# Optimization experiments

Hardware: AMD Instinct MI355X
Metric: run time of the kernel (lower is better)

The kernel has to match this reference:

```python
import jax, jax.numpy as jnp
import numpy as np

B, L, K = 2, 1024, 30
NUM_RBF = 16
MAX_REL = 32  # max_relative_feature
POS_DIM = 16

# atom order in stacked table: N=0, Ca=1, C=2, O=3, Cb=4
_PAIRS = [(0,0),(2,2),(3,3),(4,4),(1,0),(1,2),(1,3),(1,4),(0,2),(0,3),(0,4),
          (4,2),(4,3),(3,2),(0,1),(2,1),(3,1),(4,1),(2,0),(3,0),(4,0),(2,4),(3,4),(2,3)]


def setup_inputs() -> dict:
    key = jax.random.key(0)
    ks = jax.random.split(key, 6)
    X = jax.random.normal(ks[0], (B, L, 4, 3), dtype=jnp.float32) * 3.0
    chain_idx = jnp.sort(jax.random.randint(ks[1], (B, L), 0, 4), axis=-1)
    mask = jnp.ones((B, L), dtype=jnp.float32)
    E_idx = jax.random.randint(ks[2], (B, L, K), 0, L)
    D_neighbors = jax.random.uniform(ks[3], (B, L, K), dtype=jnp.float32) * 22.0
    W_pos = jax.random.normal(ks[4], (POS_DIM, 2 * MAX_REL + 2), dtype=jnp.float32) * 0.1
    b_pos = jax.random.normal(ks[5], (POS_DIM,), dtype=jnp.float32) * 0.01
    return {"X": X, "chain_idx": chain_idx, "mask": mask, "E_idx": E_idx,
            "D_neighbors": D_neighbors, "W_pos": W_pos, "b_pos": b_pos}


def _rbf(D):
    # D: [..., ] -> [..., NUM_RBF]
    D_mu = jnp.linspace(2.0, 22.0, NUM_RBF, dtype=D.dtype)
    D_sigma = (22.0 - 2.0) / NUM_RBF
    return jnp.exp(-(((D[..., None] - D_mu) / D_sigma) ** 2))


def _residue_idx(chain_idx):
    # faithful to the torch loop: chains 0..n-2 get 100*(chain#) + global pos, last chain stays -100
    boundary = jnp.concatenate(
        [jnp.zeros((chain_idx.shape[0], 1), jnp.int32),
         (chain_idx[:, 1:] != chain_idx[:, :-1]).astype(jnp.int32)], axis=1)
    chain_num = jnp.cumsum(boundary, axis=1)              # [B,L]
    last = chain_num[:, -1:]
    pos = jnp.arange(chain_idx.shape[1], dtype=jnp.int32)[None, :]
    return jnp.where(chain_num < last, 100 * chain_num + pos, -100)


def _forward(X, chain_idx, mask, E_idx, D_neighbors, W_pos, b_pos):
    N, Ca, C, O = X[:, :, 0], X[:, :, 1], X[:, :, 2], X[:, :, 3]
    b = Ca - N
    c = C - Ca
    a = jnp.cross(b, c)
    Cb = -0.58273431 * a + 0.56802827 * b - 0.54067466 * c + Ca
    atoms = jnp.stack([N, Ca, C, O, Cb], axis=0)          # [5,B,L,3]

    ia = jnp.array([p[0] for p in _PAIRS])
    ib = jnp.array([p[1] for p in _PAIRS])

    def pair_rbf(A_pts, B_pts):
        # full pairwise distance then gather down to top-k neighbors (faithful to original)
        dX = A_pts[:, :, None, :] - B_pts[:, None, :, :]   # [B,L,L,3]
        D = jnp.sqrt(jnp.sum(dX ** 2, axis=-1) + 1e-6)     # [B,L,L]
        Dn = jnp.take_along_axis(D, E_idx, axis=2)         # [B,L,K]
        return _rbf(Dn)                                     # [B,L,K,16]

    RBF_pairs = jax.vmap(pair_rbf)(atoms[ia], atoms[ib])   # [24,B,L,K,16]
    RBF_pairs = jnp.transpose(RBF_pairs, (1, 2, 3, 0, 4)).reshape(
        X.shape[0], X.shape[1], E_idx.shape[2], 24 * NUM_RBF)
    RBF_all = jnp.concatenate([_rbf(D_neighbors), RBF_pairs], axis=-1)  # [B,L,K,400]

    ridx = _residue_idx(chain_idx)                          # [B,L] int32
    offset = ridx[:, :, None] - ridx[:, None, :]            # [B,L,L]
    offset = jnp.take_along_axis(offset, E_idx, axis=2)     # [B,L,K]
    d_chains = (chain_idx[:, :, None] == chain_idx[:, None, :]).astype(jnp.int32)
    E_chains = jnp.take_along_axis(d_chains, E_idx, axis=2)  # [B,L,K]

    d = jnp.clip(offset + MAX_REL, 0, 2 * MAX_REL) * E_chains + (1 - E_chains) * (2 * MAX_REL + 1)
    d_onehot = jax.nn.one_hot(d, 2 * MAX_REL + 2, dtype=W_pos.dtype)   # [B,L,K,66]
    E_positional = jnp.einsum('blkc,ec->blke', d_onehot, W_pos) + b_pos

    return jnp.concatenate([E_positional, RBF_all], axis=-1)  # [B,L,K,416]


def reference(X, chain_idx, mask, E_idx, D_neighbors, W_pos, b_pos):
    return _forward(X, chain_idx, mask, E_idx, D_neighbors, W_pos, b_pos)
```

## Files before the change

### kernel.cpp

```cpp
#include <hip/hip_runtime.h>

#define BB 2
#define LL 1024
#define KK 30
#define NCH 416
#define PER_BLOCK (KK * NCH)
#define NF4 (PER_BLOCK / 4)

__device__ __constant__ unsigned char PAIR_A[24] =
    {0,2,3,4,1,1,1,1,0,0,0,4,4,3,0,2,3,4,2,3,4,2,3,2};
__device__ __constant__ unsigned char PAIR_B[24] =
    {0,2,3,4,0,2,3,4,2,3,4,2,3,2,1,1,1,1,0,0,0,4,4,3};

__global__ __launch_bounds__(256)
void feat_fused(const float* __restrict__ X, const int* __restrict__ chainG,
                const int* __restrict__ E_idx, const float* __restrict__ D_neighbors,
                const float* __restrict__ W_pos, const float* __restrict__ b_pos,
                float* __restrict__ out)
{
    __shared__ float Wlds[16 * 66];
    __shared__ float bpos[16];
    __shared__ float latm[16];
    __shared__ float natm[KK][16];
    __shared__ float pd[KK][26];
    __shared__ int   dd[KK];
    __shared__ int   iaib[24];
    __shared__ int   wmask[4];

    const int tid = threadIdx.x;
    const int bi  = blockIdx.x;
    const int l   = bi & (LL - 1);
    const int rowbase = bi - l;

    const int4 cv = reinterpret_cast<const int4*>(chainG + rowbase)[tid];
    int pm = (1 << cv.x) | (1 << cv.y) | (1 << cv.z) | (1 << cv.w);
    #pragma unroll
    for (int off = 32; off >= 1; off >>= 1) pm |= __shfl_xor(pm, off, 64);
    if ((tid & 63) == 0) wmask[tid >> 6] = pm;

    for (int i = tid; i < 16 * 66; i += 256) Wlds[i] = W_pos[i];
    if (tid < 16) bpos[tid] = b_pos[tid];
    if (tid < 24) iaib[tid] = ((int)(3 * PAIR_A[tid]) << 8) | (int)(3 * PAIR_B[tid]);

    int jj = 0, chj = 0;
    if (tid < KK) {
        jj  = E_idx[bi * KK + tid];
        chj = chainG[rowbase + jj];
        pd[tid][0] = D_neighbors[bi * KK + tid] * 0.8f;
    }
    if (tid <= KK) {
        const int j = (tid < KK) ? (rowbase + jj) : bi;
        const float4* xp = reinterpret_cast<const float4*>(X + (size_t)j * 12);
        const float4 x0 = xp[0], x1 = xp[1], x2 = xp[2];
        const float bx = x0.w - x0.x, by = x1.x - x0.y, bz = x1.y - x0.z;
        const float cx = x1.z - x0.w, cy = x1.w - x1.x, cz = x2.x - x1.y;
        const float ax = by * cz - bz * cy;
        const float ay = bz * cx - bx * cz;
        const float az = bx * cy - by * cx;
        const float ka = -0.58273431f, kb = 0.56802827f, kc = -0.54067466f;
        float* ap = (tid < KK) ? &natm[tid][0] : &latm[0];
        ap[0]  = x0.x; ap[1]  = x0.y; ap[2]  = x0.z;
        ap[3]  = x0.w; ap[4]  = x1.x; ap[5]  = x1.y;
        ap[6]  = x1.z; ap[7]  = x1.w; ap[8]  = x2.x;
        ap[9]  = x2.y; ap[10] = x2.z; ap[11] = x2.w;
        ap[12] = ka * ax + kb * bx + kc * cx + x0.w;
        ap[13] = ka * ay + kb * by + kc * cy + x1.x;
        ap[14] = ka * az + kb * bz + kc * cz + x1.y;
    }
    __syncthreads();

    if (tid < KK) {
        const int mask = wmask[0] | wmask[1] | wmask[2] | wmask[3];
        const int chl  = chainG[bi];
        const int npres = __popc(mask);
        const int cl1 = __popc(mask & ((2 << chl) - 1));
        const int cj1 = __popc(mask & ((2 << chj) - 1));
        const int rl = (cl1 < npres) ? (100 * (cl1 - 1) + l)  : -100;
        const int rj = (cj1 < npres) ? (100 * (cj1 - 1) + jj) : -100;
        int off = rl - rj + 32;
        off = off < 0 ? 0 : (off > 64 ? 64 : off);
        dd[tid] = (chl == chj) ? off : 65;
    }

    for (int i = tid; i < KK * 24; i += 256) {
        const int k  = i / 24;
        const int p  = i - k * 24;
        const int pk = iaib[p];
        const int ao = pk >> 8;
        const int bo = pk & 255;
        const float dx = latm[ao]     - natm[k][bo];
        const float dy = latm[ao + 1] - natm[k][bo + 1];
        const float dz = latm[ao + 2] - natm[k][bo + 2];
        const float D  = sqrtf(dx * dx + dy * dy + dz * dz + 1e-6f);
        pd[k][1 + p] = D * 0.8f;
    }
    __syncthreads();

    float* outp = out + (size_t)bi * PER_BLOCK;
    const float MU0    = 1.6f;
    const float MUSTEP = 1.0666666666666667f;
    const float NLOG2E = -1.44269504088896f;

    for (int i4 = tid; i4 < NF4; i4 += 256) {
        const int k  = i4 / 104;
        const int c0 = (i4 - k * 104) * 4;
        float4 v;
        if (c0 < 16) {
            const int d = dd[k];
            v.x = Wlds[(c0 + 0) * 66 + d] + bpos[c0 + 0];
            v.y = Wlds[(c0 + 1) * 66 + d] + bpos[c0 + 1];
            v.z = Wlds[(c0 + 2) * 66 + d] + bpos[c0 + 2];
            v.w = Wlds[(c0 + 3) * 66 + d] + bpos[c0 + 3];
        } else {
            const int q  = (c0 - 16) >> 4;
            const int m0 = (c0 - 16) & 15;
            const float D8 = pd[k][q];
            const float t0 = D8 - (MU0 + (float)(m0 + 0) * MUSTEP);
            const float t1 = D8 - (MU0 + (float)(m0 + 1) * MUSTEP);
            const float t2 = D8 - (MU0 + (float)(m0 + 2) * MUSTEP);
            const float t3 = D8 - (MU0 + (float)(m0 + 3) * MUSTEP);
            v.x = __builtin_amdgcn_exp2f(t0 * t0 * NLOG2E);
            v.y = __builtin_amdgcn_exp2f(t1 * t1 * NLOG2E);
            v.z = __builtin_amdgcn_exp2f(t2 * t2 * NLOG2E);
            v.w = __builtin_amdgcn_exp2f(t3 * t3 * NLOG2E);
        }
        *reinterpret_cast<float4*>(outp + i4 * 4) = v;
    }
}

extern "C" void kernel_launch(void* const* d_in, const int* in_sizes, int n_in,
                              void* d_out, int out_size, void* d_ws, size_t ws_size,
                              hipStream_t stream)
{
    const float* X           = (const float*)d_in[0];
    const int*   chain_idx   = (const int*)  d_in[1];
    const int*   E_idx       = (const int*)  d_in[3];
    const float* D_neighbors = (const float*)d_in[4];
    const float* W_pos       = (const float*)d_in[5];
    const float* b_pos       = (const float*)d_in[6];
    float* out = (float*)d_out;

    feat_fused<<<BB * LL, 256, 0, stream>>>(X, chain_idx, E_idx, D_neighbors,
                                            W_pos, b_pos, out);
}
```

Before: 25.12 us.

## Process two residue positions per block and split positional/RBF output loops

Each block now handles two consecutive positions, which halves the grid and amortizes the per-block setup (W_pos load, chain mask reduction) across twice the output. The chain array is cached in shared memory, and the bias is folded into the W table when it is loaded. The positional-embedding stores are split out from the RBF loop, which removes the per-element branch. The cost is more setup work and shared memory per block, fewer blocks in flight, and a dead leftover read of dd.

```diff
diff --git a/kernel.cpp b/kernel.cpp
--- a/kernel.cpp
+++ b/kernel.cpp
@@ -4,127 +4,185 @@
 #define LL 1024
 #define KK 30
 #define NCH 416
-#define PER_BLOCK (KK * NCH)
-#define NF4 (PER_BLOCK / 4)
+#define PER_POS (KK * NCH)
+#define RBF4 3000
+#define POS4 120
 
 __device__ __constant__ unsigned char PAIR_A[24] =
     {0,2,3,4,1,1,1,1,0,0,0,4,4,3,0,2,3,4,2,3,4,2,3,2};
 __device__ __constant__ unsigned char PAIR_B[24] =
     {0,2,3,4,0,2,3,4,2,3,4,2,3,2,1,1,1,1,0,0,0,4,4,3};
 
+__device__ __forceinline__ void build_atoms(float* ap, float4 x0, float4 x1, float4 x2)
+{
+    const float bx = x0.w - x0.x, by = x1.x - x0.y, bz = x1.y - x0.z;
+    const float cx = x1.z - x0.w, cy = x1.w - x1.x, cz = x2.x - x1.y;
+    const float ax = by * cz - bz * cy;
+    const float ay = bz * cx - bx * cz;
+    const float az = bx * cy - by * cx;
+    const float ka = -0.58273431f, kb = 0.56802827f, kc = -0.54067466f;
+    ap[0]  = x0.x; ap[1]  = x0.y; ap[2]  = x0.z;
+    ap[3]  = x0.w; ap[4]  = x1.x; ap[5]  = x1.y;
+    ap[6]  = x1.z; ap[7]  = x1.w; ap[8]  = x2.x;
+    ap[9]  = x2.y; ap[10] = x2.z; ap[11] = x2.w;
+    ap[12] = ka * ax + kb * bx + kc * cx + x0.w;
+    ap[13] = ka * ay + kb * by + kc * cy + x1.x;
+    ap[14] = ka * az + kb * bz + kc * cz + x1.y;
+}
+
 __global__ __launch_bounds__(256)
-void feat_fused(const float* __restrict__ X, const int* __restrict__ chainG,
-                const int* __restrict__ E_idx, const float* __restrict__ D_neighbors,
-                const float* __restrict__ W_pos, const float* __restrict__ b_pos,
-                float* __restrict__ out)
+void feat_fused2(const float* __restrict__ X, const int* __restrict__ chainG,
+                 const int* __restrict__ E_idx, const float* __restrict__ D_neighbors,
+                 const float* __restrict__ W_pos, const float* __restrict__ b_pos,
+                 float* __restrict__ out)
 {
-    __shared__ float Wlds[16 * 66];
-    __shared__ float bpos[16];
-    __shared__ float latm[16];
-    __shared__ float natm[KK][16];
-    __shared__ float pd[KK][26];
-    __shared__ int   dd[KK];
+    __shared__ float Wst[16 * 66];
+    __shared__ int   schain[LL];
+    __shared__ float latm[2][16];
+    __shared__ float natm[2][KK][16];
+    __shared__ float pd[2][KK][26];
+    __shared__ int   dd[2][KK];
     __shared__ int   iaib[24];
     __shared__ int   wmask[4];
 
     const int tid = threadIdx.x;
-    const int bi  = blockIdx.x;
-    const int l   = bi & (LL - 1);
-    const int rowbase = bi - l;
-
-    const int4 cv = reinterpret_cast<const int4*>(chainG + rowbase)[tid];
-    int pm = (1 << cv.x) | (1 << cv.y) | (1 << cv.z) | (1 << cv.w);
+    const int p0  = blockIdx.x * 2;
+    const int p1  = p0 + 1;
+    const int l0  = p0 & (LL - 1);
+    const int l1  = l0 + 1;
+    const int rowbase = p0 - l0;
+
+    const int4 cvv = reinterpret_cast<const int4*>(chainG + rowbase)[tid];
+    reinterpret_cast<int4*>(schain)[tid] = cvv;
+    int pm = (1 << cvv.x) | (1 << cvv.y) | (1 << cvv.z) | (1 << cvv.w);
     #pragma unroll
     for (int off = 32; off >= 1; off >>= 1) pm |= __shfl_xor(pm, off, 64);
     if ((tid & 63) == 0) wmask[tid >> 6] = pm;
 
-    for (int i = tid; i < 16 * 66; i += 256) Wlds[i] = W_pos[i];
-    if (tid < 16) bpos[tid] = b_pos[tid];
+    for (int i = tid; i < 16 * 66; i += 256) Wst[i] = W_pos[i] + b_pos[i / 66];
     if (tid < 24) iaib[tid] = ((int)(3 * PAIR_A[tid]) << 8) | (int)(3 * PAIR_B[tid]);
 
-    int jj = 0, chj = 0;
+    int jj0 = 0, jj1 = 0;
     if (tid < KK) {
-        jj  = E_idx[bi * KK + tid];
-        chj = chainG[rowbase + jj];
-        pd[tid][0] = D_neighbors[bi * KK + tid] * 0.8f;
+        jj0 = E_idx[p0 * KK + tid];
+        jj1 = E_idx[p1 * KK + tid];
+        pd[0][tid][0] = D_neighbors[p0 * KK + tid] * 0.8f;
+        pd[1][tid][0] = D_neighbors[p1 * KK + tid] * 0.8f;
     }
     if (tid <= KK) {
-        const int j = (tid < KK) ? (rowbase + jj) : bi;
-        const float4* xp = reinterpret_cast<const float4*>(X + (size_t)j * 12);
-        const float4 x0 = xp[0], x1 = xp[1], x2 = xp[2];
-        const float bx = x0.w - x0.x, by = x1.x - x0.y, bz = x1.y - x0.z;
-        const float cx = x1.z - x0.w, cy = x1.w - x1.x, cz = x2.x - x1.y;
-        const float ax = by * cz - bz * cy;
-        const float ay = bz * cx - bx * cz;
-        const float az = bx * cy - by * cx;
-        const float ka = -0.58273431f, kb = 0.56802827f, kc = -0.54067466f;
-        float* ap = (tid < KK) ? &natm[tid][0] : &latm[0];
-        ap[0]  = x0.x; ap[1]  = x0.y; ap[2]  = x0.z;
-        ap[3]  = x0.w; ap[4]  = x1.x; ap[5]  = x1.y;
-        ap[6]  = x1.z; ap[7]  = x1.w; ap[8]  = x2.x;
-        ap[9]  = x2.y; ap[10] = x2.z; ap[11] = x2.w;
-        ap[12] = ka * ax + kb * bx + kc * cx + x0.w;
-        ap[13] = ka * ay + kb * by + kc * cy + x1.x;
-        ap[14] = ka * az + kb * bz + kc * cz + x1.y;
+        const int j0 = (tid < KK) ? (rowbase + jj0) : p0;
+        const int j1 = (tid < KK) ? (rowbase + jj1) : p1;
+        const float4* q0 = reinterpret_cast<const float4*>(X + (size_t)j0 * 12);
+        const float4* q1 = reinterpret_cast<const float4*>(X + (size_t)j1 * 12);
+        const float4 a0 = q0[0], a1 = q0[1], a2 = q0[2];
+        const float4 b0 = q1[0], b1 = q1[1], b2 = q1[2];
+        build_atoms((tid < KK) ? &natm[0][tid][0] : &latm[0][0], a0, a1, a2);
+        build_atoms((tid < KK) ? &natm[1][tid][0] : &latm[1][0], b0, b1, b2);
     }
     __syncthreads();
 
     if (tid < KK) {
-        const int mask = wmask[0] | wmask[1] | wmask[2] | wmask[3];
-        const int chl  = chainG[bi];
+        const int mask  = wmask[0] | wmask[1] | wmask[2] | wmask[3];
         const int npres = __popc(mask);
-        const int cl1 = __popc(mask & ((2 << chl) - 1));
-        const int cj1 = __popc(mask & ((2 << chj) - 1));
-        const int rl = (cl1 < npres) ? (100 * (cl1 - 1) + l)  : -100;
-        const int rj = (cj1 < npres) ? (100 * (cj1 - 1) + jj) : -100;
-        int off = rl - rj + 32;
-        off = off < 0 ? 0 : (off > 64 ? 64 : off);
-        dd[tid] = (chl == chj) ? off : 65;
-    }
-
-    for (int i = tid; i < KK * 24; i += 256) {
-        const int k  = i / 24;
-        const int p  = i - k * 24;
-        const int pk = iaib[p];
-        const int ao = pk >> 8;
-        const int bo = pk & 255;
-        const float dx = latm[ao]     - natm[k][bo];
-        const float dy = latm[ao + 1] - natm[k][bo + 1];
-        const float dz = latm[ao + 2] - natm[k][bo + 2];
+        {
+            const int chl = schain[l0], chj = schain[jj0];
+            const int cl1 = __popc(mask & ((2 << chl) - 1));
+            const int cj1 = __popc(mask & ((2 << chj) - 1));
+            const int rl = (cl1 < npres) ? (100 * (cl1 - 1) + l0)  : -100;
+            const int rj = (cj1 < npres) ? (100 * (cj1 - 1) + jj0) : -100;
+            int off = rl - rj + 32;
+            off = off < 0 ? 0 : (off > 64 ? 64 : off);
+            dd[0][tid] = (chl == chj) ? off : 65;
+        }
+        {
+            const int chl = schain[l1], chj = schain[jj1];
+            const int cl1 = __popc(mask & ((2 << chl) - 1));
+            const int cj1 = __popc(mask & ((2 << chj) - 1));
+            const int rl = (cl1 < npres) ? (100 * (cl1 - 1) + l1)  : -100;
+            const int rj = (cj1 < npres) ? (100 * (cj1 - 1) + jj1) : -100;
+            int off = rl - rj + 32;
+            off = off < 0 ? 0 : (off > 64 ? 64 : off);
+            dd[1][tid] = (chl == chj) ? off : 65;
+        }
+    }
+
+    for (int i = tid; i < 2 * KK * 24; i += 256) {
+        const int g   = (i >= KK * 24);
+        const int rem = i - g * (KK * 24);
+        const int k   = rem / 24;
+        const int p   = rem - k * 24;
+        const int pk  = iaib[p];
+        const int ao  = pk >> 8;
+        const int bo  = pk & 255;
+        const float dx = latm[g][ao]     - natm[g][k][bo];
+        const float dy = latm[g][ao + 1] - natm[g][k][bo + 1];
+        const float dz = latm[g][ao + 2] - natm[g][k][bo + 2];
         const float D  = sqrtf(dx * dx + dy * dy + dz * dz + 1e-6f);
-        pd[k][1 + p] = D * 0.8f;
+        pd[g][k][1 + p] = D * 0.8f;
     }
     __syncthreads();
 
-    float* outp = out + (size_t)bi * PER_BLOCK;
+    float* outp0 = out + (size_t)p0 * PER_POS;
+    float* outp1 = outp0 + PER_POS;
+
+    if (tid < 2 * POS4) {
+        const int g   = (tid >= POS4);
+        const int rem = tid - g * POS4;
+        const int k   = rem >> 2;
+        const int c0  = (rem & 3) * 4;
+        const int d   = dd[g][tid >> 2 & 31];
+        (void)d;
+        const int dv  = dd[g][k];
+        float4 v;
+        v.x = Wst[(c0 + 0) * 66 + dv];
+        v.y = Wst[(c0 + 1) * 66 + dv];
+        v.z = Wst[(c0 + 2) * 66 + dv];
+        v.w = Wst[(c0 + 3) * 66 + dv];
+        float* op = g ? outp1 : outp0;
+        *reinterpret_cast<float4*>(op + k * NCH + c0) = v;
+    }
+
     const float MU0    = 1.6f;
     const float MUSTEP = 1.0666666666666667f;
     const float NLOG2E = -1.44269504088896f;
 
-    for (int i4 = tid; i4 < NF4; i4 += 256) {
-        const int k  = i4 / 104;
-        const int c0 = (i4 - k * 104) * 4;
+    #pragma unroll 1
+    for (int i4 = tid; i4 < RBF4; i4 += 256) {
+        const int k    = i4 / 100;
+        const int rem4 = i4 - k * 100;
+        const int q    = rem4 >> 2;
+        const int m0   = (rem4 & 3) << 2;
+        const float D8 = pd[0][k][q];
+        const float mu = MU0 + (float)m0 * MUSTEP;
+        const float t0 = D8 - mu;
+        const float t1 = D8 - (mu + MUSTEP);
+        const float t2 = D8 - (mu + 2.0f * MUSTEP);
+        const float t3 = D8 - (mu + 3.0f * MUSTEP);
         float4 v;
-        if (c0 < 16) {
-            const int d = dd[k];
-            v.x = Wlds[(c0 + 0) * 66 + d] + bpos[c0 + 0];
-            v.y = Wlds[(c0 + 1) * 66 + d] + bpos[c0 + 1];
-            v.z = Wlds[(c0 + 2) * 66 + d] + bpos[c0 + 2];
-            v.w = Wlds[(c0 + 3) * 66 + d] + bpos[c0 + 3];
-        } else {
-            const int q  = (c0 - 16) >> 4;
-            const int m0 = (c0 - 16) & 15;
-            const float D8 = pd[k][q];
-            const float t0 = D8 - (MU0 + (float)(m0 + 0) * MUSTEP);
-            const float t1 = D8 - (MU0 + (float)(m0 + 1) * MUSTEP);
-            const float t2 = D8 - (MU0 + (float)(m0 + 2) * MUSTEP);
-            const float t3 = D8 - (MU0 + (float)(m0 + 3) * MUSTEP);
-            v.x = __builtin_amdgcn_exp2f(t0 * t0 * NLOG2E);
-            v.y = __builtin_amdgcn_exp2f(t1 * t1 * NLOG2E);
-            v.z = __builtin_amdgcn_exp2f(t2 * t2 * NLOG2E);
-            v.w = __builtin_amdgcn_exp2f(t3 * t3 * NLOG2E);
-        }
-        *reinterpret_cast<float4*>(outp + i4 * 4) = v;
+        v.x = __builtin_amdgcn_exp2f(t0 * t0 * NLOG2E);
+        v.y = __builtin_amdgcn_exp2f(t1 * t1 * NLOG2E);
+        v.z = __builtin_amdgcn_exp2f(t2 * t2 * NLOG2E);
+        v.w = __builtin_amdgcn_exp2f(t3 * t3 * NLOG2E);
+        *reinterpret_cast<float4*>(outp0 + k * NCH + 16 + rem4 * 4) = v;
+    }
+    #pragma unroll 1
+    for (int i4 = tid; i4 < RBF4; i4 += 256) {
+        const int k    = i4 / 100;
+        const int rem4 = i4 - k * 100;
+        const int q    = rem4 >> 2;
+        const int m0   = (rem4 & 3) << 2;
+        const float D8 = pd[1][k][q];
+        const float mu = MU0 + (float)m0 * MUSTEP;
+        const float t0 = D8 - mu;
+        const float t1 = D8 - (mu + MUSTEP);
+        const float t2 = D8 - (mu + 2.0f * MUSTEP);
+        const float t3 = D8 - (mu + 3.0f * MUSTEP);
+        float4 v;
+        v.x = __builtin_amdgcn_exp2f(t0 * t0 * NLOG2E);
+        v.y = __builtin_amdgcn_exp2f(t1 * t1 * NLOG2E);
+        v.z = __builtin_amdgcn_exp2f(t2 * t2 * NLOG2E);
+        v.w = __builtin_amdgcn_exp2f(t3 * t3 * NLOG2E);
+        *reinterpret_cast<float4*>(outp1 + k * NCH + 16 + rem4 * 4) = v;
     }
 }
 
@@ -140,6 +198,6 @@
     const float* b_pos       = (const float*)d_in[6];
     float* out = (float*)d_out;
 
-    feat_fused<<<BB * LL, 256, 0, stream>>>(X, chain_idx, E_idx, D_neighbors,
-                                            W_pos, b_pos, out);
+    feat_fused2<<<(BB * LL) / 2, 256, 0, stream>>>(X, chain_idx, E_idx,
+                                                   D_neighbors, W_pos, b_pos, out);
 }
```

After: 26.02 us. 3.6% more time.

## Split each position's neighbors across six blocks to raise parallelism

Applied to the files above, without the earlier changes.

Each block now handles 5 of the 30 neighbors for one position instead of all 30, so the grid grows sixfold and each block's output loop becomes three fixed emits. The bias is folded into the staged W table, removing one add per positional output. The cost is that every block repeats the per-row work: loading W_pos into shared memory, the chain-mask reduction over 1024 chain ids, and building the center residue's atoms.

```diff
diff --git a/kernel.cpp b/kernel.cpp
--- a/kernel.cpp
+++ b/kernel.cpp
@@ -4,75 +4,84 @@
 #define LL 1024
 #define KK 30
 #define NCH 416
-#define PER_BLOCK (KK * NCH)
-#define NF4 (PER_BLOCK / 4)
+#define PER_POS (KK * NCH)
+#define KC 5
+#define NBPP (KK / KC)
+#define WF4 (KC * 104)
 
 __device__ __constant__ unsigned char PAIR_A[24] =
     {0,2,3,4,1,1,1,1,0,0,0,4,4,3,0,2,3,4,2,3,4,2,3,2};
 __device__ __constant__ unsigned char PAIR_B[24] =
     {0,2,3,4,0,2,3,4,2,3,4,2,3,2,1,1,1,1,0,0,0,4,4,3};
 
+__device__ __forceinline__ void build_atoms(float* ap, float4 x0, float4 x1, float4 x2)
+{
+    const float bx = x0.w - x0.x, by = x1.x - x0.y, bz = x1.y - x0.z;
+    const float cx = x1.z - x0.w, cy = x1.w - x1.x, cz = x2.x - x1.y;
+    const float ax = by * cz - bz * cy;
+    const float ay = bz * cx - bx * cz;
+    const float az = bx * cy - by * cx;
+    const float ka = -0.58273431f, kb = 0.56802827f, kc = -0.54067466f;
+    ap[0]  = x0.x; ap[1]  = x0.y; ap[2]  = x0.z;
+    ap[3]  = x0.w; ap[4]  = x1.x; ap[5]  = x1.y;
+    ap[6]  = x1.z; ap[7]  = x1.w; ap[8]  = x2.x;
+    ap[9]  = x2.y; ap[10] = x2.z; ap[11] = x2.w;
+    ap[12] = ka * ax + kb * bx + kc * cx + x0.w;
+    ap[13] = ka * ay + kb * by + kc * cy + x1.x;
+    ap[14] = ka * az + kb * bz + kc * cz + x1.y;
+}
+
 __global__ __launch_bounds__(256)
-void feat_fused(const float* __restrict__ X, const int* __restrict__ chainG,
+void feat_split(const float* __restrict__ X, const int* __restrict__ chainG,
                 const int* __restrict__ E_idx, const float* __restrict__ D_neighbors,
                 const float* __restrict__ W_pos, const float* __restrict__ b_pos,
                 float* __restrict__ out)
 {
-    __shared__ float Wlds[16 * 66];
-    __shared__ float bpos[16];
+    __shared__ float Wst[16 * 66];
     __shared__ float latm[16];
-    __shared__ float natm[KK][16];
-    __shared__ float pd[KK][26];
-    __shared__ int   dd[KK];
+    __shared__ float natm[KC][16];
+    __shared__ float pd[KC][26];
+    __shared__ int   dd[KC];
     __shared__ int   iaib[24];
     __shared__ int   wmask[4];
 
     const int tid = threadIdx.x;
-    const int bi  = blockIdx.x;
-    const int l   = bi & (LL - 1);
-    const int rowbase = bi - l;
+    const int bid = blockIdx.x;
+    const int pos = bid / NBPP;
+    const int kc  = bid - pos * NBPP;
+    const int k0  = kc * KC;
+    const int l   = pos & (LL - 1);
+    const int rowbase = pos - l;
 
-    const int4 cv = reinterpret_cast<const int4*>(chainG + rowbase)[tid];
-    int pm = (1 << cv.x) | (1 << cv.y) | (1 << cv.z) | (1 << cv.w);
-    #pragma unroll
-    for (int off = 32; off >= 1; off >>= 1) pm |= __shfl_xor(pm, off, 64);
-    if ((tid & 63) == 0) wmask[tid >> 6] = pm;
+    int jj = 0, chj = 0;
+    if (tid < KC) {
+        jj  = E_idx[pos * KK + k0 + tid];
+        chj = chainG[rowbase + jj];
+        pd[tid][0] = D_neighbors[pos * KK + k0 + tid] * 0.8f;
+    }
+    if (tid <= KC) {
+        const int j = (tid < KC) ? (rowbase + jj) : pos;
+        const float4* xp = reinterpret_cast<const float4*>(X + (size_t)j * 12);
+        const float4 x0 = xp[0], x1 = xp[1], x2 = xp[2];
+        build_atoms((tid < KC) ? &natm[tid][0] : &latm[0], x0, x1, x2);
+    }
 
-    for (int i = tid; i < 16 * 66; i += 256) Wlds[i] = W_pos[i];
-    if (tid < 16) bpos[tid] = b_pos[tid];
+    for (int i = tid; i < 16 * 66; i += 256) Wst[i] = W_pos[i] + b_pos[i / 66];
     if (tid < 24) iaib[tid] = ((int)(3 * PAIR_A[tid]) << 8) | (int)(3 * PAIR_B[tid]);
 
-    int jj = 0, chj = 0;
-    if (tid < KK) {
-        jj  = E_idx[bi * KK + tid];
-        chj = chainG[rowbase + jj];
-        pd[tid][0] = D_neighbors[bi * KK + tid] * 0.8f;
-    }
-    if (tid <= KK) {
-        const int j = (tid < KK) ? (rowbase + jj) : bi;
-        const float4* xp = reinterpret_cast<const float4*>(X + (size_t)j * 12);
-        const float4 x0 = xp[0], x1 = xp[1], x2 = xp[2];
-        const float bx = x0.w - x0.x, by = x1.x - x0.y, bz = x1.y - x0.z;
-        const float cx = x1.z - x0.w, cy = x1.w - x1.x, cz = x2.x - x1.y;
-        const float ax = by * cz - bz * cy;
-        const float ay = bz * cx - bx * cz;
-        const float az = bx * cy - by * cx;
-        const float ka = -0.58273431f, kb = 0.56802827f, kc = -0.54067466f;
-        float* ap = (tid < KK) ? &natm[tid][0] : &latm[0];
-        ap[0]  = x0.x; ap[1]  = x0.y; ap[2]  = x0.z;
-        ap[3]  = x0.w; ap[4]  = x1.x; ap[5]  = x1.y;
-        ap[6]  = x1.z; ap[7]  = x1.w; ap[8]  = x2.x;
-        ap[9]  = x2.y; ap[10] = x2.z; ap[11] = x2.w;
-        ap[12] = ka * ax + kb * bx + kc * cx + x0.w;
-        ap[13] = ka * ay + kb * by + kc * cy + x1.x;
-        ap[14] = ka * az + kb * bz + kc * cz + x1.y;
+    {
+        const int4 cv = reinterpret_cast<const int4*>(chainG + rowbase)[tid];
+        int pm = (1 << cv.x) | (1 << cv.y) | (1 << cv.z) | (1 << cv.w);
+        #pragma unroll
+        for (int off = 32; off >= 1; off >>= 1) pm |= __shfl_xor(pm, off, 64);
+        if ((tid & 63) == 0) wmask[tid >> 6] = pm;
     }
     __syncthreads();
 
-    if (tid < KK) {
-        const int mask = wmask[0] | wmask[1] | wmask[2] | wmask[3];
-        const int chl  = chainG[bi];
+    if (tid < KC) {
+        const int mask  = wmask[0] | wmask[1] | wmask[2] | wmask[3];
         const int npres = __popc(mask);
+        const int chl   = chainG[pos];
         const int cl1 = __popc(mask & ((2 << chl) - 1));
         const int cj1 = __popc(mask & ((2 << chj) - 1));
         const int rl = (cl1 < npres) ? (100 * (cl1 - 1) + l)  : -100;
@@ -82,9 +91,9 @@
         dd[tid] = (chl == chj) ? off : 65;
     }
 
-    for (int i = tid; i < KK * 24; i += 256) {
-        const int k  = i / 24;
-        const int p  = i - k * 24;
+    if (tid < KC * 24) {
+        const int k  = tid / 24;
+        const int p  = tid - k * 24;
         const int pk = iaib[p];
         const int ao = pk >> 8;
         const int bo = pk & 255;
@@ -96,36 +105,41 @@
     }
     __syncthreads();
 
-    float* outp = out + (size_t)bi * PER_BLOCK;
+    float* outp = out + (size_t)pos * PER_POS + (size_t)k0 * NCH;
     const float MU0    = 1.6f;
     const float MUSTEP = 1.0666666666666667f;
     const float NLOG2E = -1.44269504088896f;
 
-    for (int i4 = tid; i4 < NF4; i4 += 256) {
+    auto emit = [&](int i4) {
         const int k  = i4 / 104;
         const int c0 = (i4 - k * 104) * 4;
         float4 v;
         if (c0 < 16) {
-            const int d = dd[k];
-            v.x = Wlds[(c0 + 0) * 66 + d] + bpos[c0 + 0];
-            v.y = Wlds[(c0 + 1) * 66 + d] + bpos[c0 + 1];
-            v.z = Wlds[(c0 + 2) * 66 + d] + bpos[c0 + 2];
-            v.w = Wlds[(c0 + 3) * 66 + d] + bpos[c0 + 3];
+            const int dv = dd[k];
+            v.x = Wst[(c0 + 0) * 66 + dv];
+            v.y = Wst[(c0 + 1) * 66 + dv];
+            v.z = Wst[(c0 + 2) * 66 + dv];
+            v.w = Wst[(c0 + 3) * 66 + dv];
         } else {
             const int q  = (c0 - 16) >> 4;
             const int m0 = (c0 - 16) & 15;
             const float D8 = pd[k][q];
-            const float t0 = D8 - (MU0 + (float)(m0 + 0) * MUSTEP);
-            const float t1 = D8 - (MU0 + (float)(m0 + 1) * MUSTEP);
-            const float t2 = D8 - (MU0 + (float)(m0 + 2) * MUSTEP);
-            const float t3 = D8 - (MU0 + (float)(m0 + 3) * MUSTEP);
+            const float mu = MU0 + (float)m0 * MUSTEP;
+            const float t0 = D8 - mu;
+            const float t1 = D8 - (mu + MUSTEP);
+            const float t2 = D8 - (mu + 2.0f * MUSTEP);
+            const float t3 = D8 - (mu + 3.0f * MUSTEP);
             v.x = __builtin_amdgcn_exp2f(t0 * t0 * NLOG2E);
             v.y = __builtin_amdgcn_exp2f(t1 * t1 * NLOG2E);
             v.z = __builtin_amdgcn_exp2f(t2 * t2 * NLOG2E);
             v.w = __builtin_amdgcn_exp2f(t3 * t3 * NLOG2E);
         }
         *reinterpret_cast<float4*>(outp + i4 * 4) = v;
-    }
+    };
+
+    emit(tid);
+    emit(tid + 256);
+    if (tid < WF4 - 512) emit(tid + 512);
 }
 
 extern "C" void kernel_launch(void* const* d_in, const int* in_sizes, int n_in,
@@ -140,6 +154,6 @@
     const float* b_pos       = (const float*)d_in[6];
     float* out = (float*)d_out;
 
-    feat_fused<<<BB * LL, 256, 0, stream>>>(X, chain_idx, E_idx, D_neighbors,
-                                            W_pos, b_pos, out);
+    feat_split<<<BB * LL * NBPP, 256, 0, stream>>>(X, chain_idx, E_idx,
+                                                   D_neighbors, W_pos, b_pos, out);
 }
```

New measurement: 31.83 us. 26.7% more time.
